# Performance work log

Measured on AMD Instinct MI355X. Metric: run time of the kernel, lower is better.

The kernel has to match this reference:

```python
import jax, jax.numpy as jnp
import numpy as np

N = 50000        # nodes
E = 800000       # edges (edge-nodes of the line graph)
LGE = 1600000    # line-graph edges
F_NODE = 256     # node feature dim
T = 64           # timestamp/edge feature dim
HID = 128        # hidden size
OUT = 64         # out size
SLOPE = 0.2      # leaky relu negative slope used in EdgeGCN / attention


def _glorot(key, shape):
    lim = jnp.sqrt(6.0 / (shape[0] + shape[1]))
    return jax.random.uniform(key, shape, jnp.float32, -lim, lim)


def setup_inputs() -> dict:
    key = jax.random.key(0)
    ks = jax.random.split(key, 24)
    inp = {
        "x": jax.random.normal(ks[0], (N, F_NODE), jnp.float32),
        "et": jax.random.normal(ks[1], (E, T), jnp.float32),
        "H": jax.random.randint(ks[2], (2, E), 0, N),
        "raw_edge_index": jax.random.randint(ks[3], (2, E), 0, N),
        "lg_edge_index": jax.random.randint(ks[4], (2, LGE), 0, E),
        # TSAEncoder: two SAGE-style layers on the line graph (T->HID->HID)
        "W_tsa1_s": _glorot(ks[5], (T, HID)),
        "W_tsa1_n": _glorot(ks[6], (T, HID)),
        "W_tsa2_s": _glorot(ks[7], (HID, HID)),
        "W_tsa2_n": _glorot(ks[8], (HID, HID)),
        # EdgeToNodeConv + EdgeGCN output linear
        "W_etn": _glorot(ks[9], (HID, HID)),
        "W_eg_lin": _glorot(ks[10], (HID, HID)),
        # edge_aggr SAGE (num_layers-1 = 1 layer)
        "W_ea_s": _glorot(ks[11], (HID, HID)),
        "W_ea_n": _glorot(ks[12], (HID, HID)),
        # attr_node_model SAGE (2 layers)
        "W_an1_s": _glorot(ks[13], (F_NODE, HID)),
        "W_an1_n": _glorot(ks[14], (F_NODE, HID)),
        "W_an2_s": _glorot(ks[15], (HID, HID)),
        "W_an2_n": _glorot(ks[16], (HID, HID)),
        # MixAttention
        "Wq": _glorot(ks[17], (HID, HID)),
        "Wk": _glorot(ks[18], (HID, HID)),
        "Wv": _glorot(ks[19], (HID, HID)),
        # final classifier
        "W_out": _glorot(ks[20], (HID, OUT)),
    }
    return inp


def _sage(h, src, dst, Ws, Wn, n):
    # mean-aggregator SAGE conv: self transform + mean of in-neighbors
    deg = jnp.clip(jax.ops.segment_sum(jnp.ones(src.shape[0], h.dtype), dst, num_segments=n), 1.0)
    nbr = jax.ops.segment_sum(h[src], dst, num_segments=n) / deg[:, None]
    return h @ Ws + nbr @ Wn


def reference(x, et, H, raw_edge_index, lg_edge_index,
              W_tsa1_s, W_tsa1_n, W_tsa2_s, W_tsa2_n,
              W_etn, W_eg_lin, W_ea_s, W_ea_n,
              W_an1_s, W_an1_n, W_an2_s, W_an2_n,
              Wq, Wk, Wv, W_out):
    src_lg, dst_lg = lg_edge_index[0], lg_edge_index[1]
    src, dst = raw_edge_index[0], raw_edge_index[1]

    # ---- EdgeGCN: TSAEncoder over line graph (edges as nodes) ----
    h = jax.nn.relu(_sage(et, src_lg, dst_lg, W_tsa1_s, W_tsa1_n, E))
    h = _sage(h, src_lg, dst_lg, W_tsa2_s, W_tsa2_n, E)          # [E, HID]

    # ---- EdgeToNodeConv: scatter edge reprs to both incident nodes (mean) ----
    ones_e = jnp.ones(E, h.dtype)
    agg = (jax.ops.segment_sum(h, H[0], num_segments=N)
           + jax.ops.segment_sum(h, H[1], num_segments=N))        # [N, HID]
    deg = jnp.clip(jax.ops.segment_sum(ones_e, H[0], num_segments=N)
                   + jax.ops.segment_sum(ones_e, H[1], num_segments=N), 1.0)
    node_e = (agg / deg[:, None]) @ W_etn
    edge_repr = jax.nn.leaky_relu(node_e, negative_slope=SLOPE) @ W_eg_lin  # [N, HID]

    # ---- edge_aggr: 1-layer SAGE over raw graph ----
    aggr_edge = _sage(edge_repr, src, dst, W_ea_s, W_ea_n, N)     # [N, HID]

    # ---- attr_node_model: 2-layer SAGE ----
    hn = jax.nn.relu(_sage(x, src, dst, W_an1_s, W_an1_n, N))
    hn = _sage(hn, src, dst, W_an2_s, W_an2_n, N)                 # [N, HID]

    # ---- MixAttention: edge-indexed cross attention (node queries, edge-repr keys/values) ----
    q = hn @ Wq
    k = aggr_edge @ Wk
    v = aggr_edge @ Wv
    score = jax.nn.leaky_relu(
        jnp.sum(q[dst] * k[src], axis=-1) / jnp.sqrt(jnp.asarray(HID, q.dtype)),
        negative_slope=SLOPE)                                     # [E]
    m = jax.ops.segment_max(score, dst, num_segments=N)
    m = jnp.where(jnp.isfinite(m), m, 0.0)
    ex = jnp.exp(score - m[dst])
    den = jnp.clip(jax.ops.segment_sum(ex, dst, num_segments=N), 1e-9)
    alpha = ex / den[dst]
    out = hn + jax.ops.segment_sum(alpha[:, None] * v[src], dst, num_segments=N)

    return jax.nn.log_softmax(out @ W_out, axis=1)                # [N, OUT]
```

## Files before the change

kernel.cpp:

```cpp
#include <hip/hip_runtime.h>
#include <cstddef>

static constexpr int Nn   = 50000;
static constexpr int Ee   = 800000;
static constexpr int LGEe = 1600000;

typedef __attribute__((ext_vector_type(8))) short bf16x8;
typedef __attribute__((ext_vector_type(4))) float f32x4;

__device__ __forceinline__ float bf2f(unsigned int u16) {
  return __uint_as_float(u16 << 16);
}
__device__ __forceinline__ unsigned int f2bf(float f) {
  unsigned int u = __float_as_uint(f);
  u += 0x7fffu + ((u >> 16) & 1u);
  return u >> 16;
}

__global__ __launch_bounds__(256)
void k_count_direct(const int* __restrict__ idx, int* __restrict__ cnt, int n) {
  int i = blockIdx.x * 256 + threadIdx.x;
  if (i < n) atomicAdd(&cnt[idx[i]], 1);
}
__global__ __launch_bounds__(256)
void k_scan1(const int* __restrict__ in, int* __restrict__ out,
             int* __restrict__ bsum, int n) {
  __shared__ int sd[256];
  int tid = threadIdx.x;
  int base = blockIdx.x * 1024 + tid * 4;
  int4 v = {0, 0, 0, 0};
  if (base < n) v = *(const int4*)(in + base);
  int s = v.x + v.y + v.z + v.w;
  sd[tid] = s; __syncthreads();
  for (int off = 1; off < 256; off <<= 1) {
    int t_ = (tid >= off) ? sd[tid - off] : 0; __syncthreads();
    sd[tid] += t_; __syncthreads();
  }
  int excl = sd[tid] - s;
  if (base < n) {
    int4 o; o.x = excl; o.y = o.x + v.x; o.z = o.y + v.y; o.w = o.z + v.z;
    *(int4*)(out + base) = o;
  }
  if (tid == 255) bsum[blockIdx.x] = sd[255];
}
__global__ __launch_bounds__(1024)
void k_scan2(int* __restrict__ b, int nb) {
  __shared__ int sd[1024];
  int tid = threadIdx.x;
  int v = (tid < nb) ? b[tid] : 0;
  sd[tid] = v; __syncthreads();
  for (int off = 1; off < 1024; off <<= 1) {
    int t_ = (tid >= off) ? sd[tid - off] : 0; __syncthreads();
    sd[tid] += t_; __syncthreads();
  }
  if (tid < nb) b[tid] = sd[tid] - v;
}
__global__ __launch_bounds__(256)
void k_scan3(int* __restrict__ out, const int* __restrict__ bsum, int n, int total,
             int* __restrict__ cur) {
  int i = blockIdx.x * 256 + threadIdx.x;
  if (i < n) {
    int v = out[i] + bsum[i >> 10];
    out[i] = v;
    cur[i] = v;
  }
  if (i == 0) out[n] = total;
}
__global__ __launch_bounds__(256)
void k_fillA(const int* __restrict__ dlg, const int* __restrict__ slg,
             int* __restrict__ cur, int* __restrict__ ent, int n) {
  int m = blockIdx.x * 256 + threadIdx.x;
  if (m >= n) return;
  int pos = atomicAdd(&cur[dlg[m]], 1);
  ent[pos] = slg[m];
}
__global__ __launch_bounds__(256)
void k_fillC2(const int* __restrict__ H, int* __restrict__ cur,
              int* __restrict__ ent, int n2, int E) {
  int i = blockIdx.x * 256 + threadIdx.x;
  if (i >= n2) return;
  int pos = atomicAdd(&cur[H[i]], 1);
  ent[pos] = (i >= E) ? i - E : i;
}
__global__ __launch_bounds__(256)
void k_fillD(const int* __restrict__ dstA, const int* __restrict__ srcA,
             int* __restrict__ cur, int* __restrict__ ent, int n) {
  int e = blockIdx.x * 256 + threadIdx.x;
  if (e >= n) return;
  int pos = atomicAdd(&cur[dstA[e]], 1);
  ent[pos] = srcA[e];
}
__global__ __launch_bounds__(256)
void k_rdeg(const int* __restrict__ ptr, float* __restrict__ r, int n) {
  int i = blockIdx.x * 256 + threadIdx.x;
  if (i < n) r[i] = 1.0f / fmaxf((float)(ptr[i + 1] - ptr[i]), 1.0f);
}

#define MG_SWEEP(WP, ACC)                                                       \
  {                                                                             \
    bf16x8 Bh[2][4], Bl[2][4];                                                  \
    _Pragma("unroll")                                                           \
    for (int np = 0; np < 2; ++np) {                                            \
      int n = (wv * 2 + np) * 16 + nrow;                                        \
      _Pragma("unroll")                                                         \
      for (int kc = 0; kc < 4; ++kc) {                                          \
        int kr0 = kh * 128 + kc * 32 + kg * 8;                                  \
        _Pragma("unroll")                                                       \
        for (int j = 0; j < 8; ++j) {                                           \
          float w = (WP)[(size_t)(kr0 + j) * 128 + n];                          \
          unsigned int hi = __float_as_uint(w) >> 16;                           \
          float lo = w - bf2f(hi);                                              \
          Bh[np][kc][j] = (short)(unsigned short)hi;                            \
          Bl[np][kc][j] = (short)(unsigned short)(__float_as_uint(lo) >> 16);   \
        }                                                                       \
      }                                                                         \
    }                                                                           \
    _Pragma("unroll")                                                           \
    for (int kc = 0; kc < 4; ++kc) {                                            \
      _Pragma("unroll")                                                         \
      for (int m = 0; m < 4; ++m) {                                             \
        int ss = m * 16 + nrow;                                                 \
        int idx = ss * 128 + ((kc * 32 + kg * 8) ^ ((ss & 7) << 3));            \
        bf16x8 ah = *(const bf16x8*)(sAh + idx);                                \
        bf16x8 al = *(const bf16x8*)(sAl + idx);                                \
        _Pragma("unroll")                                                       \
        for (int np = 0; np < 2; ++np) {                                        \
          ACC[m][np] = __builtin_amdgcn_mfma_f32_16x16x32_bf16(ah, Bh[np][kc], ACC[m][np], 0, 0, 0); \
          ACC[m][np] = __builtin_amdgcn_mfma_f32_16x16x32_bf16(al, Bh[np][kc], ACC[m][np], 0, 0, 0); \
          ACC[m][np] = __builtin_amdgcn_mfma_f32_16x16x32_bf16(ah, Bl[np][kc], ACC[m][np], 0, 0, 0); \
        }                                                                       \
      }                                                                         \
    }                                                                           \
  }

template <int DUAL>
__global__ __launch_bounds__(256)
void k_mgemm(int M, const float* __restrict__ A, int K,
             const float* __restrict__ W1, const float* __restrict__ W2,
             const float* __restrict__ dgA, int reluA, int act,
             float* __restrict__ C1, float* __restrict__ C2, int beta1)
{
  __shared__ __align__(16) unsigned char smem[34816];
  unsigned short* sAh = (unsigned short*)smem;
  unsigned short* sAl = (unsigned short*)(smem + 16384);
  float* stage = (float*)smem;

  const int t = threadIdx.x, wv = t >> 6;
  const int tr = t >> 4, tc = t & 15;
  const int nrow = (t & 63) & 15, kg = (t & 63) >> 4;
  const int row0 = blockIdx.x * 64;

  f32x4 acc1[4][2], acc2[4][2];
  #pragma unroll
  for (int m = 0; m < 4; ++m)
    #pragma unroll
    for (int np = 0; np < 2; ++np) {
      acc1[m][np] = (f32x4){0.f, 0.f, 0.f, 0.f};
      if (DUAL) acc2[m][np] = (f32x4){0.f, 0.f, 0.f, 0.f};
    }

  const int nkh = K >> 7;
  #pragma unroll 1
  for (int kh = 0; kh < nkh; ++kh) {
    if (kh) __syncthreads();
    #pragma unroll
    for (int j = 0; j < 8; ++j) {
      int idx = t + j * 256;
      int r = idx >> 5, c4 = idx & 31;
      int gr = row0 + r; if (gr > M - 1) gr = M - 1;
      float4 va = *(const float4*)(A + (size_t)gr * K + kh * 128 + c4 * 4);
      if (reluA) {
        va.x = fmaxf(va.x, 0.f); va.y = fmaxf(va.y, 0.f);
        va.z = fmaxf(va.z, 0.f); va.w = fmaxf(va.w, 0.f);
      }
      if (dgA) {
        float sc = dgA[gr];
        va.x *= sc; va.y *= sc; va.z *= sc; va.w *= sc;
      }
      float v[4] = {va.x, va.y, va.z, va.w};
      unsigned int h[4], l[4];
      #pragma unroll
      for (int q = 0; q < 4; ++q) {
        h[q] = __float_as_uint(v[q]) >> 16;
        l[q] = __float_as_uint(v[q] - bf2f(h[q])) >> 16;
      }
      int bidx = r * 128 + ((c4 * 4) ^ ((r & 7) << 3));
      uint2 ph = {h[0] | (h[1] << 16), h[2] | (h[3] << 16)};
      uint2 pl = {l[0] | (l[1] << 16), l[2] | (l[3] << 16)};
      *(uint2*)(sAh + bidx) = ph;
      *(uint2*)(sAl + bidx) = pl;
    }
    __syncthreads();

    MG_SWEEP(W1, acc1);
    if (DUAL) MG_SWEEP(W2, acc2);
  }

  __syncthreads();
  #pragma unroll
  for (int m = 0; m < 4; ++m)
    #pragma unroll
    for (int np = 0; np < 2; ++np)
      #pragma unroll
      for (int r = 0; r < 4; ++r)
        stage[(m * 16 + kg * 4 + r) * 132 + (wv * 2 + np) * 16 + nrow] = acc1[m][np][r];
  __syncthreads();
  #pragma unroll
  for (int i = 0; i < 4; ++i) {
    int s = tr * 4 + i, gr = row0 + s;
    if (gr >= M) continue;
    const float* sp = stage + s * 132 + tc * 8;
    float4 v0 = *(const float4*)sp, v1 = *(const float4*)(sp + 4);
    float o[8] = {v0.x, v0.y, v0.z, v0.w, v1.x, v1.y, v1.z, v1.w};
    #pragma unroll
    for (int j2 = 0; j2 < 8; ++j2) {
      float vv = o[j2];
      if (act == 1)      vv = fmaxf(vv, 0.f);
      else if (act == 2) vv = vv > 0.f ? vv : 0.2f * vv;
      o[j2] = vv;
    }
    float* p = C1 + (size_t)gr * 128 + tc * 8;
    if (beta1) {
      float4 c0 = *(const float4*)p, c1 = *(const float4*)(p + 4);
      o[0] += c0.x; o[1] += c0.y; o[2] += c0.z; o[3] += c0.w;
      o[4] += c1.x; o[5] += c1.y; o[6] += c1.z; o[7] += c1.w;
    }
    *(float4*)p       = *(const float4*)&o[0];
    *(float4*)(p + 4) = *(const float4*)&o[4];
  }
  if (DUAL) {
    __syncthreads();
    #pragma unroll
    for (int m = 0; m < 4; ++m)
      #pragma unroll
      for (int np = 0; np < 2; ++np)
        #pragma unroll
        for (int r = 0; r < 4; ++r)
          stage[(m * 16 + kg * 4 + r) * 132 + (wv * 2 + np) * 16 + nrow] = acc2[m][np][r];
    __syncthreads();
    #pragma unroll
    for (int i = 0; i < 4; ++i) {
      int s = tr * 4 + i, gr = row0 + s;
      if (gr >= M) continue;
      const float* sp = stage + s * 132 + tc * 8;
      float4 v0 = *(const float4*)sp, v1 = *(const float4*)(sp + 4);
      float o[8] = {v0.x, v0.y, v0.z, v0.w, v1.x, v1.y, v1.z, v1.w};
      #pragma unroll
      for (int j2 = 0; j2 < 8; ++j2) {
        float vv = o[j2];
        if (act == 1)      vv = fmaxf(vv, 0.f);
        else if (act == 2) vv = vv > 0.f ? vv : 0.2f * vv;
        o[j2] = vv;
      }
      float* p = C2 + (size_t)gr * 128 + tc * 8;
      *(float4*)p       = *(const float4*)&o[0];
      *(float4*)(p + 4) = *(const float4*)&o[4];
    }
  }
}

__global__ __launch_bounds__(256)
void k_tsa1(const float* __restrict__ et,
            const int* __restrict__ rp, const int* __restrict__ ent,
            const float* __restrict__ Ws, const float* __restrict__ Wn,
            unsigned short* __restrict__ BUF)
{
  __shared__ __align__(16) unsigned char smem[34816];
  unsigned short* sAh = (unsigned short*)smem;
  unsigned short* sAl = (unsigned short*)(smem + 16384);
  int*   sEnt  = (int*)(smem + 32768);
  float* stage = (float*)smem;

  const int t = threadIdx.x, wv = t >> 6, lane = t & 63;
  const int tr = t >> 4, tc = t & 15;
  const int nrow = lane & 15, kg = lane >> 4;
  const int seg0 = blockIdx.x * 64;
  const int segbase = seg0 + wv * 16;

  int rpv = (lane <= 16) ? rp[segbase + lane] : 0;
  int nxtv = __shfl(rpv, (lane + 1) & 63);
  float invv = 1.f / fmaxf((float)(nxtv - rpv), 1.f);

  const int base = rp[seg0];
  const int cnt  = rp[seg0 + 64] - base;
  const int lim  = cnt < 512 ? cnt : 512;
  for (int i = t; i < lim; i += 256) sEnt[i] = ent[base + i];

  {
    float dv[16];
    #pragma unroll
    for (int i = 0; i < 16; ++i)
      dv[i] = et[(size_t)(segbase + i) * 64 + lane];
    #pragma unroll
    for (int i = 0; i < 16; ++i) {
      int ss = wv * 16 + i;
      unsigned int hi = __float_as_uint(dv[i]) >> 16;
      float lo = dv[i] - bf2f(hi);
      int idx = ss * 128 + (lane ^ ((ss & 7) << 3));
      sAh[idx] = (unsigned short)hi;
      sAl[idx] = (unsigned short)(__float_as_uint(lo) >> 16);
    }
  }

  bf16x8 Bh[2][4], Bl[2][4];
  #pragma unroll
  for (int np = 0; np < 2; ++np) {
    int n = (wv * 2 + np) * 16 + nrow;
    #pragma unroll
    for (int kc = 0; kc < 4; ++kc) {
      const float* Wp = (kc < 2) ? Ws : Wn;
      int kr0 = (kc & 1) * 32 + kg * 8;
      #pragma unroll
      for (int j = 0; j < 8; ++j) {
        float w = Wp[(size_t)(kr0 + j) * 128 + n];
        unsigned int hi = __float_as_uint(w) >> 16;
        float lo = w - bf2f(hi);
        Bh[np][kc][j] = (short)(unsigned short)hi;
        Bl[np][kc][j] = (short)(unsigned short)(__float_as_uint(lo) >> 16);
      }
    }
  }
  __syncthreads();

  {
    int q0 = __shfl(rpv, 0);
    int q1 = __shfl(rpv, 16);
    int c = 0;
    int b_next = __shfl(rpv, 1);
    float idg = __shfl(invv, 0);
    float a = 0.f;
    #pragma unroll 1
    for (int j = q0; j < q1; j += 8) {
      float x[8];
      #pragma unroll
      for (int u = 0; u < 8; ++u) {
        int jj = j + u; jj = jj < q1 ? jj : q1 - 1;
        int ix = jj - base;
        int s = (ix < 512) ? sEnt[ix] : ent[jj];
        x[u] = et[(size_t)s * 64 + lane];
      }
      #pragma unroll
      for (int u = 0; u < 8; ++u) {
        int jj = j + u;
        if (jj >= q1) break;
        while (jj >= b_next) {
          float v = a * idg;
          int ss = wv * 16 + c;
          unsigned int hi = __float_as_uint(v) >> 16;
          float lo = v - bf2f(hi);
          int idx = ss * 128 + ((64 + lane) ^ ((ss & 7) << 3));
          sAh[idx] = (unsigned short)hi;
          sAl[idx] = (unsigned short)(__float_as_uint(lo) >> 16);
          a = 0.f;
          ++c;
          b_next = __shfl(rpv, c + 1);
          idg = __shfl(invv, c);
        }
        a += x[u];
      }
    }
    #pragma unroll 1
    for (;;) {
      float v = a * idg;
      int ss = wv * 16 + c;
      unsigned int hi = __float_as_uint(v) >> 16;
      float lo = v - bf2f(hi);
      int idx = ss * 128 + ((64 + lane) ^ ((ss & 7) << 3));
      sAh[idx] = (unsigned short)hi;
      sAl[idx] = (unsigned short)(__float_as_uint(lo) >> 16);
      a = 0.f;
      if (++c >= 16) break;
      idg = __shfl(invv, c);
    }
  }
  __syncthreads();

  f32x4 acc[4][2];
  #pragma unroll
  for (int m = 0; m < 4; ++m)
    #pragma unroll
    for (int np = 0; np < 2; ++np)
      acc[m][np] = (f32x4){0.f, 0.f, 0.f, 0.f};

  #pragma unroll
  for (int kc = 0; kc < 4; ++kc) {
    #pragma unroll
    for (int m = 0; m < 4; ++m) {
      int ss = m * 16 + nrow;
      int kbase = kc * 32 + kg * 8;
      int idx = ss * 128 + (kbase ^ ((ss & 7) << 3));
      bf16x8 ah = *(const bf16x8*)(sAh + idx);
      bf16x8 al = *(const bf16x8*)(sAl + idx);
      #pragma unroll
      for (int np = 0; np < 2; ++np) {
        acc[m][np] = __builtin_amdgcn_mfma_f32_16x16x32_bf16(ah, Bh[np][kc], acc[m][np], 0, 0, 0);
        acc[m][np] = __builtin_amdgcn_mfma_f32_16x16x32_bf16(al, Bh[np][kc], acc[m][np], 0, 0, 0);
        acc[m][np] = __builtin_amdgcn_mfma_f32_16x16x32_bf16(ah, Bl[np][kc], acc[m][np], 0, 0, 0);
      }
    }
  }

  __syncthreads();
  #pragma unroll
  for (int m = 0; m < 4; ++m)
    #pragma unroll
    for (int np = 0; np < 2; ++np)
      #pragma unroll
      for (int r = 0; r < 4; ++r)
        stage[(m * 16 + kg * 4 + r) * 132 + (wv * 2 + np) * 16 + nrow] = acc[m][np][r];
  __syncthreads();
  #pragma unroll
  for (int i = 0; i < 4; ++i) {
    int s = tr * 4 + i;
    const float* sp = stage + s * 132 + tc * 8;
    float4 v0 = *(const float4*)sp;
    float4 v1 = *(const float4*)(sp + 4);
    unsigned int pk[4];
    pk[0] = f2bf(v0.x) | (f2bf(v0.y) << 16);
    pk[1] = f2bf(v0.z) | (f2bf(v0.w) << 16);
    pk[2] = f2bf(v1.x) | (f2bf(v1.y) << 16);
    pk[3] = f2bf(v1.z) | (f2bf(v1.w) << 16);
    uint4 st = {pk[0], pk[1], pk[2], pk[3]};
    *(uint4*)(BUF + (size_t)(seg0 + s) * 128 + tc * 8) = st;
  }
}

__global__ __launch_bounds__(256)
void k_pool12(const int* __restrict__ rp, const int* __restrict__ ent,
              const int* __restrict__ rpA, const int* __restrict__ entA,
              const unsigned short* __restrict__ BUF,
              float* __restrict__ OS, float* __restrict__ ON,
              int nseg, int total)
{
  const int wv = threadIdx.x >> 6, lane = threadIdx.x & 63;
  const int chunk = blockIdx.x * 4 + wv;
  const int c0 = chunk * 128;
  if (c0 >= total) return;
  int c1 = c0 + 128; if (c1 > total) c1 = total;

  int lo = 0, hi = nseg;
  while (lo + 1 < hi) {
    int mid = (lo + hi) >> 1;
    if (rp[mid] <= c0) lo = mid; else hi = mid;
  }
  int seg = lo;
  int sstart = rp[seg];
  int send = rp[seg + 1];
  float s0 = 0.f, s1 = 0.f, n0 = 0.f, n1 = 0.f;

  #pragma unroll 1
  for (int j = c0; j < c1; j += 8) {
    int ids[8];
    #pragma unroll
    for (int u = 0; u < 8; ++u) {
      int jj = j + u; jj = jj < c1 ? jj : c1 - 1;
      ids[u] = ent[jj];
    }
    unsigned int uv[8];
    int pA0[8], pA1[8];
    #pragma unroll
    for (int u = 0; u < 8; ++u)
      uv[u] = *(const unsigned int*)(BUF + (size_t)ids[u] * 128 + 2 * lane);
    #pragma unroll
    for (int u = 0; u < 8; ++u) { pA0[u] = rpA[ids[u]]; pA1[u] = rpA[ids[u] + 1]; }
    #pragma unroll
    for (int u = 0; u < 8; ++u) {
      int jj = j + u;
      if (jj >= c1) break;
      while (jj >= send) {
        float* pS = OS + (size_t)seg * 128;
        float* pN = ON + (size_t)seg * 128;
        if (sstart >= c0 && send <= c1) {
          pS[2 * lane]     += s0;  pS[2 * lane + 1] += s1;
          pN[2 * lane]     += n0;  pN[2 * lane + 1] += n1;
        } else {
          atomicAdd(pS + 2 * lane, s0);     atomicAdd(pS + 2 * lane + 1, s1);
          atomicAdd(pN + 2 * lane, n0);     atomicAdd(pN + 2 * lane + 1, n1);
        }
        s0 = s1 = n0 = n1 = 0.f;
        ++seg; sstart = send; send = rp[seg + 1];
      }
      s0 += fmaxf(bf2f(uv[u] & 0xffffu), 0.f);
      s1 += fmaxf(bf2f(uv[u] >> 16),     0.f);
      int p0 = pA0[u], p1 = pA1[u];
      float a0 = 0.f, a1 = 0.f;
      #pragma unroll 1
      for (int t2 = p0; t2 < p1; t2 += 4) {
        unsigned int w[4];
        int rem = p1 - t2;
        #pragma unroll
        for (int v2 = 0; v2 < 4; ++v2)
          if (v2 < rem)
            w[v2] = *(const unsigned int*)(BUF + (size_t)entA[t2 + v2] * 128 + 2 * lane);
        #pragma unroll
        for (int v2 = 0; v2 < 4; ++v2)
          if (v2 < rem) {
            a0 += fmaxf(bf2f(w[v2] & 0xffffu), 0.f);
            a1 += fmaxf(bf2f(w[v2] >> 16),     0.f);
          }
      }
      float idg = 1.f / fmaxf((float)(p1 - p0), 1.f);
      n0 += a0 * idg; n1 += a1 * idg;
    }
  }
  {
    float* pS = OS + (size_t)seg * 128;
    float* pN = ON + (size_t)seg * 128;
    if (sstart >= c0 && send <= c1) {
      pS[2 * lane]     += s0;  pS[2 * lane + 1] += s1;
      pN[2 * lane]     += n0;  pN[2 * lane + 1] += n1;
    } else {
      atomicAdd(pS + 2 * lane, s0);     atomicAdd(pS + 2 * lane + 1, s1);
      atomicAdd(pN + 2 * lane, n0);     atomicAdd(pN + 2 * lane + 1, n1);
    }
  }
}

__global__ __launch_bounds__(256)
void k_poolf(const int* __restrict__ rp, const int* __restrict__ ent,
             const float* __restrict__ SRC, float* __restrict__ O,
             int nseg, int total)
{
  const int wv = threadIdx.x >> 6, lane = threadIdx.x & 63;
  const int chunk = blockIdx.x * 4 + wv;
  const int c0 = chunk * 256;
  if (c0 >= total) return;
  int c1 = c0 + 256; if (c1 > total) c1 = total;

  int lo = 0, hi = nseg;
  while (lo + 1 < hi) {
    int mid = (lo + hi) >> 1;
    if (rp[mid] <= c0) lo = mid; else hi = mid;
  }
  int seg = lo;
  int sstart = rp[seg];
  int send = rp[seg + 1];
  float a0 = 0.f, a1 = 0.f;

  #pragma unroll 1
  for (int j = c0; j < c1; j += 8) {
    int ids[8];
    #pragma unroll
    for (int u = 0; u < 8; ++u) {
      int jj = j + u; jj = jj < c1 ? jj : c1 - 1;
      ids[u] = ent[jj];
    }
    float2 v[8];
    #pragma unroll
    for (int u = 0; u < 8; ++u)
      v[u] = ((const float2*)(SRC + (size_t)ids[u] * 128))[lane];
    #pragma unroll
    for (int u = 0; u < 8; ++u) {
      int jj = j + u;
      if (jj >= c1) break;
      while (jj >= send) {
        float sc = 1.f / fmaxf((float)(send - sstart), 1.f);
        float* p = O + (size_t)seg * 128;
        if (sstart >= c0 && send <= c1) {
          p[2 * lane]     += a0 * sc;
          p[2 * lane + 1] += a1 * sc;
        } else {
          atomicAdd(p + 2 * lane, a0 * sc);
          atomicAdd(p + 2 * lane + 1, a1 * sc);
        }
        a0 = a1 = 0.f;
        ++seg; sstart = send; send = rp[seg + 1];
      }
      a0 += v[u].x; a1 += v[u].y;
    }
  }
  {
    float sc = 1.f / fmaxf((float)(send - sstart), 1.f);
    float* p = O + (size_t)seg * 128;
    if (sstart >= c0 && send <= c1) {
      p[2 * lane]     += a0 * sc;
      p[2 * lane + 1] += a1 * sc;
    } else {
      atomicAdd(p + 2 * lane, a0 * sc);
      atomicAdd(p + 2 * lane + 1, a1 * sc);
    }
  }
}

__global__ __launch_bounds__(256)
void k_attn(const int* __restrict__ rp, const int* __restrict__ ent,
            const float* __restrict__ q, const float* __restrict__ kb,
            const float* __restrict__ vb, float* __restrict__ o, int nseg)
{
  int wv = threadIdx.x >> 6, lane = threadIdx.x & 63;
  int seg = blockIdx.x * 4 + wv;
  if (seg >= nseg) return;
  int p0 = rp[seg], p1 = rp[seg + 1];
  if (p0 >= p1) return;
  float2 q2 = ((const float2*)(q + (size_t)seg * 128))[lane];
  float m = -1e30f, l = 0.f, o0 = 0.f, o1 = 0.f;
  #pragma unroll 1
  for (int j = p0; j < p1; j += 4) {
    int s[4];
    #pragma unroll
    for (int i = 0; i < 4; ++i) {
      int jj = j + i; jj = jj < p1 ? jj : p1 - 1;
      s[i] = ent[jj];
    }
    float2 k2[4], v2[4];
    #pragma unroll
    for (int i = 0; i < 4; ++i)
      k2[i] = ((const float2*)(kb + (size_t)s[i] * 128))[lane];
    #pragma unroll
    for (int i = 0; i < 4; ++i)
      v2[i] = ((const float2*)(vb + (size_t)s[i] * 128))[lane];
    float d[4];
    #pragma unroll
    for (int i = 0; i < 4; ++i) d[i] = fmaf(q2.x, k2[i].x, q2.y * k2[i].y);
    #pragma unroll
    for (int off = 1; off < 64; off <<= 1) {
      #pragma unroll
      for (int i = 0; i < 4; ++i) d[i] += __shfl_xor(d[i], off);
    }
    float sc[4];
    #pragma unroll
    for (int i = 0; i < 4; ++i) {
      float v = d[i] * 0.088388347648318447f;
      v = v > 0.f ? v : 0.2f * v;
      sc[i] = (j + i < p1) ? v : -1e30f;
    }
    float mb = fmaxf(fmaxf(sc[0], sc[1]), fmaxf(sc[2], sc[3]));
    float mn = fmaxf(m, mb);
    float scale = expf(m - mn);
    float e[4];
    #pragma unroll
    for (int i = 0; i < 4; ++i)
      e[i] = (j + i < p1) ? expf(sc[i] - mn) : 0.f;
    l  = l  * scale + ((e[0] + e[1]) + (e[2] + e[3]));
    o0 = o0 * scale + ((e[0] * v2[0].x + e[1] * v2[1].x) + (e[2] * v2[2].x + e[3] * v2[3].x));
    o1 = o1 * scale + ((e[0] * v2[0].y + e[1] * v2[1].y) + (e[2] * v2[2].y + e[3] * v2[3].y));
    m = mn;
  }
  float inv = 1.f / fmaxf(l, 1e-9f);
  float2* orow = (float2*)(o + (size_t)seg * 128);
  float2 cur = orow[lane];
  cur.x += o0 * inv; cur.y += o1 * inv;
  orow[lane] = cur;
}

__global__ __launch_bounds__(256)
void k_out(const float* __restrict__ attn, const float* __restrict__ Wout,
           float* __restrict__ out, int n) {
  __shared__ float sW[128 * 64];
  for (int i = threadIdx.x; i < 128 * 64; i += 256) sW[i] = Wout[i];
  __syncthreads();
  int wave = threadIdx.x >> 6, lane = threadIdx.x & 63;
  int row = blockIdx.x * 4 + wave;
  if (row >= n) return;
  const float* a = attn + (size_t)row * 128;
  float z = 0.f;
  #pragma unroll 8
  for (int k = 0; k < 128; ++k) z = fmaf(a[k], sW[k * 64 + lane], z);
  float mx = z;
  #pragma unroll
  for (int off = 32; off; off >>= 1) mx = fmaxf(mx, __shfl_xor(mx, off));
  float ee = expf(z - mx);
  float ss = ee;
  #pragma unroll
  for (int off = 32; off; off >>= 1) ss += __shfl_xor(ss, off);
  out[(size_t)row * 64 + lane] = z - mx - logf(ss);
}

extern "C" void kernel_launch(void* const* d_in, const int* in_sizes, int n_in,
                              void* d_out, int out_size, void* d_ws, size_t ws_size,
                              hipStream_t stream) {
  (void)in_sizes; (void)n_in; (void)out_size;
  const float* x        = (const float*)d_in[0];
  const float* et       = (const float*)d_in[1];
  const int*   H0       = (const int*)d_in[2];
  const int*   src      = (const int*)d_in[3];
  const int*   dst      = src + Ee;
  const int*   src_lg   = (const int*)d_in[4];
  const int*   dst_lg   = src_lg + LGEe;
  const float* W_tsa1_s = (const float*)d_in[5];
  const float* W_tsa1_n = (const float*)d_in[6];
  const float* W_tsa2_s = (const float*)d_in[7];
  const float* W_tsa2_n = (const float*)d_in[8];
  const float* W_etn    = (const float*)d_in[9];
  const float* W_eg_lin = (const float*)d_in[10];
  const float* W_ea_s   = (const float*)d_in[11];
  const float* W_ea_n   = (const float*)d_in[12];
  const float* W_an1_s  = (const float*)d_in[13];
  const float* W_an1_n  = (const float*)d_in[14];
  const float* W_an2_s  = (const float*)d_in[15];
  const float* W_an2_n  = (const float*)d_in[16];
  const float* Wq       = (const float*)d_in[17];
  const float* Wk       = (const float*)d_in[18];
  const float* Wv       = (const float*)d_in[19];
  const float* W_out    = (const float*)d_in[20];
  float* out = (float*)d_out;

  char* wp = (char*)d_ws;
  size_t avail = ws_size;
  auto alloc = [&](size_t bytes) -> void* {
    void* r = (void*)wp;
    size_t pad = (bytes + 255) & ~(size_t)255;
    wp += pad; avail = (avail >= pad) ? avail - pad : 0;
    return r;
  };
  const size_t NH = (size_t)Nn * 128;
  unsigned short* BUF = (unsigned short*)alloc((size_t)Ee * 128 * 2);
  float* aggN  = (float*)alloc(NH * 4);
  float* aggS  = (float*)alloc(NH * 4);
  int* ptrA  = (int*)alloc(((size_t)Ee + 1) * 4);
  int* cntA  = (int*)alloc((size_t)Ee * 4);
  int* entA  = (int*)alloc((size_t)LGEe * 4);
  int* ptrC  = (int*)alloc(((size_t)Nn + 1) * 4);
  int* cntC  = (int*)alloc((size_t)Nn * 4);
  int* entC  = (int*)alloc((size_t)2 * Ee * 4);
  int* ptrD  = (int*)alloc(((size_t)Nn + 1) * 4);
  int* cntD  = (int*)alloc((size_t)Nn * 4);
  int* entD  = (int*)alloc((size_t)Ee * 4);
  float* rdegN = (float*)alloc((size_t)Nn * 4);
  int* bsum  = (int*)alloc(2048 * 4);
  if (avail == 0 && wp > (char*)d_ws + ws_size) return;

  float* er  = (float*)BUF + 0 * NH;
  float* ae  = (float*)BUF + 1 * NH;
  float* hn  = (float*)BUF + 2 * NH;
  float* hn2 = (float*)BUF + 3 * NH;
  float* qb  = (float*)BUF + 4 * NH;
  float* kb  = (float*)BUF + 5 * NH;
  float* vb  = (float*)BUF + 6 * NH;
  float* tmp = (float*)BUF + 7 * NH;

  auto cdiv = [](long a, long b) { return (int)((a + b - 1) / b); };
  auto scan = [&](int* cnt, int* ptr, int n, int total) {
    int nb = cdiv(n, 1024);
    k_scan1<<<nb, 256, 0, stream>>>(cnt, ptr, bsum, n);
    k_scan2<<<1, 1024, 0, stream>>>(bsum, nb);
    k_scan3<<<cdiv(n, 256), 256, 0, stream>>>(ptr, bsum, n, total, cnt);
  };

  const int gLG = cdiv(LGEe, 256), gEe = cdiv(Ee, 256), g2E = cdiv(2 * Ee, 256);

  hipMemsetAsync(cntA, 0, (size_t)Ee * 4, stream);
  k_count_direct<<<gLG, 256, 0, stream>>>(dst_lg, cntA, LGEe);
  scan(cntA, ptrA, Ee, LGEe);
  k_fillA<<<gLG, 256, 0, stream>>>(dst_lg, src_lg, cntA, entA, LGEe);

  hipMemsetAsync(cntC, 0, (size_t)Nn * 4, stream);
  k_count_direct<<<g2E, 256, 0, stream>>>(H0, cntC, 2 * Ee);
  scan(cntC, ptrC, Nn, 2 * Ee);
  k_fillC2<<<g2E, 256, 0, stream>>>(H0, cntC, entC, 2 * Ee, Ee);

  hipMemsetAsync(cntD, 0, (size_t)Nn * 4, stream);
  k_count_direct<<<gEe, 256, 0, stream>>>(dst, cntD, Ee);
  scan(cntD, ptrD, Nn, Ee);
  k_fillD<<<gEe, 256, 0, stream>>>(dst, src, cntD, entD, Ee);
  k_rdeg<<<cdiv(Nn, 256), 256, 0, stream>>>(ptrC, rdegN, Nn);

  const int gM64  = cdiv(Nn, 64);
  const int gW    = cdiv(Nn, 4);
  const int gP12  = cdiv(cdiv(2 * Ee, 128), 4);
  const int gPf   = cdiv(cdiv(Ee, 256), 4);

  k_tsa1<<<Ee / 64, 256, 0, stream>>>(et, ptrA, entA, W_tsa1_s, W_tsa1_n, BUF);

  hipMemsetAsync(aggS, 0, NH * 4, stream);
  hipMemsetAsync(aggN, 0, NH * 4, stream);
  k_pool12<<<gP12, 256, 0, stream>>>(ptrC, entC, ptrA, entA, BUF, aggS, aggN, Nn, 2 * Ee);
  k_mgemm<0><<<gM64, 256, 0, stream>>>(Nn, aggN, 128, W_tsa2_n, nullptr, nullptr, 0, 0, aggN, nullptr, 0);
  k_mgemm<0><<<gM64, 256, 0, stream>>>(Nn, aggS, 128, W_tsa2_s, nullptr, nullptr, 0, 0, aggN, nullptr, 1);
  k_mgemm<0><<<gM64, 256, 0, stream>>>(Nn, aggN, 128, W_etn, nullptr, rdegN, 0, 2, tmp, nullptr, 0);
  k_mgemm<0><<<gM64, 256, 0, stream>>>(Nn, tmp, 128, W_eg_lin, nullptr, nullptr, 0, 0, er, nullptr, 0);

  k_mgemm<1><<<gM64, 256, 0, stream>>>(Nn, er, 128, W_ea_s, W_ea_n, nullptr, 0, 0, ae, tmp, 0);
  k_poolf<<<gPf, 256, 0, stream>>>(ptrD, entD, tmp, ae, Nn, Ee);

  k_mgemm<1><<<gM64, 256, 0, stream>>>(Nn, x, 256, W_an1_s, W_an1_n, nullptr, 0, 0, hn, tmp, 0);
  k_poolf<<<gPf, 256, 0, stream>>>(ptrD, entD, tmp, hn, Nn, Ee);
  k_mgemm<1><<<gM64, 256, 0, stream>>>(Nn, hn, 128, W_an2_s, W_an2_n, nullptr, 1, 0, hn2, tmp, 0);
  k_poolf<<<gPf, 256, 0, stream>>>(ptrD, entD, tmp, hn2, Nn, Ee);

  k_mgemm<0><<<gM64, 256, 0, stream>>>(Nn, hn2, 128, Wq, nullptr, nullptr, 0, 0, qb, nullptr, 0);
  k_mgemm<1><<<gM64, 256, 0, stream>>>(Nn, ae, 128, Wk, Wv, nullptr, 0, 0, kb, vb, 0);
  k_attn<<<gW, 256, 0, stream>>>(ptrD, entD, qb, kb, vb, hn2, Nn);

  k_out<<<gW, 256, 0, stream>>>(hn2, W_out, out, Nn);
}
```

Measured before the change: 2.356 ms.

## Precompute flattened composed CSR for two-hop neighbor pooling with per-entry weights

Replaces the nested two-level gather in the fused pool kernel, which walked each incident edge's line-graph neighbor list, with a precomputed CSR that maps each node directly to line-graph source edges, each carrying a 1/deg weight. Pooling then becomes two flat weighted segment-sum passes using a single generic kernel. This removes the irregular inner loop and its load imbalance. In exchange it adds a count/scan/fill pass over 3.2M entries with atomics, plus about 25MB of extra index and weight arrays.

```diff
diff --git a/kernel.cpp b/kernel.cpp
--- a/kernel.cpp
+++ b/kernel.cpp
@@ -21,6 +21,15 @@
 void k_count_direct(const int* __restrict__ idx, int* __restrict__ cnt, int n) {
   int i = blockIdx.x * 256 + threadIdx.x;
   if (i < n) atomicAdd(&cnt[idx[i]], 1);
+}
+__global__ __launch_bounds__(256)
+void k_count_comp2(const int* __restrict__ H, const int* __restrict__ dlg,
+                   int* __restrict__ cnt, int n2, int LGE, int E) {
+  int i = blockIdx.x * 256 + threadIdx.x;
+  if (i >= n2) return;
+  int b = i >= LGE;
+  int m = b ? i - LGE : i;
+  atomicAdd(&cnt[H[b * E + dlg[m]]], 1);
 }
 __global__ __launch_bounds__(256)
 void k_scan1(const int* __restrict__ in, int* __restrict__ out,
@@ -73,6 +82,21 @@
   if (m >= n) return;
   int pos = atomicAdd(&cur[dlg[m]], 1);
   ent[pos] = slg[m];
+}
+__global__ __launch_bounds__(256)
+void k_fillB2(const int* __restrict__ H, const int* __restrict__ dlg,
+              const int* __restrict__ slg, const int* __restrict__ ptrA,
+              int* __restrict__ cur, int* __restrict__ entS,
+              float* __restrict__ entW, int n2, int LGE, int E) {
+  int i = blockIdx.x * 256 + threadIdx.x;
+  if (i >= n2) return;
+  int b = i >= LGE;
+  int m = b ? i - LGE : i;
+  int d = dlg[m];
+  int pos = atomicAdd(&cur[H[b * E + d]], 1);
+  entS[pos] = slg[m];
+  int la = ptrA[d + 1] - ptrA[d];
+  entW[pos] = 1.0f / (float)max(la, 1);
 }
 __global__ __launch_bounds__(256)
 void k_fillC2(const int* __restrict__ H, int* __restrict__ cur,
@@ -426,17 +450,16 @@
 }
 
 __global__ __launch_bounds__(256)
-void k_pool12(const int* __restrict__ rp, const int* __restrict__ ent,
-              const int* __restrict__ rpA, const int* __restrict__ entA,
-              const unsigned short* __restrict__ BUF,
-              float* __restrict__ OS, float* __restrict__ ON,
-              int nseg, int total)
+void k_poolb(const int* __restrict__ rp, const int* __restrict__ ent,
+             const float* __restrict__ entw,
+             const unsigned short* __restrict__ SRC,
+             float* __restrict__ O, int nseg, int total)
 {
   const int wv = threadIdx.x >> 6, lane = threadIdx.x & 63;
   const int chunk = blockIdx.x * 4 + wv;
-  const int c0 = chunk * 128;
+  const int c0 = chunk * 256;
   if (c0 >= total) return;
-  int c1 = c0 + 128; if (c1 > total) c1 = total;
+  int c1 = c0 + 256; if (c1 > total) c1 = total;
 
   int lo = 0, hi = nseg;
   while (lo + 1 < hi) {
@@ -446,72 +469,49 @@
   int seg = lo;
   int sstart = rp[seg];
   int send = rp[seg + 1];
-  float s0 = 0.f, s1 = 0.f, n0 = 0.f, n1 = 0.f;
+  float a0 = 0.f, a1 = 0.f;
 
   #pragma unroll 1
   for (int j = c0; j < c1; j += 8) {
-    int ids[8];
+    int ids[8]; float w[8];
     #pragma unroll
     for (int u = 0; u < 8; ++u) {
       int jj = j + u; jj = jj < c1 ? jj : c1 - 1;
       ids[u] = ent[jj];
+      w[u] = entw ? entw[jj] : 1.f;
     }
     unsigned int uv[8];
-    int pA0[8], pA1[8];
     #pragma unroll
     for (int u = 0; u < 8; ++u)
-      uv[u] = *(const unsigned int*)(BUF + (size_t)ids[u] * 128 + 2 * lane);
-    #pragma unroll
-    for (int u = 0; u < 8; ++u) { pA0[u] = rpA[ids[u]]; pA1[u] = rpA[ids[u] + 1]; }
+      uv[u] = *(const unsigned int*)(SRC + (size_t)ids[u] * 128 + 2 * lane);
     #pragma unroll
     for (int u = 0; u < 8; ++u) {
       int jj = j + u;
       if (jj >= c1) break;
       while (jj >= send) {
-        float* pS = OS + (size_t)seg * 128;
-        float* pN = ON + (size_t)seg * 128;
+        float* p = O + (size_t)seg * 128;
         if (sstart >= c0 && send <= c1) {
-          pS[2 * lane]     += s0;  pS[2 * lane + 1] += s1;
-          pN[2 * lane]     += n0;  pN[2 * lane + 1] += n1;
+          p[2 * lane]     += a0;
+          p[2 * lane + 1] += a1;
         } else {
-          atomicAdd(pS + 2 * lane, s0);     atomicAdd(pS + 2 * lane + 1, s1);
-          atomicAdd(pN + 2 * lane, n0);     atomicAdd(pN + 2 * lane + 1, n1);
+          atomicAdd(p + 2 * lane, a0);
+          atomicAdd(p + 2 * lane + 1, a1);
         }
-        s0 = s1 = n0 = n1 = 0.f;
+        a0 = a1 = 0.f;
         ++seg; sstart = send; send = rp[seg + 1];
       }
-      s0 += fmaxf(bf2f(uv[u] & 0xffffu), 0.f);
-      s1 += fmaxf(bf2f(uv[u] >> 16),     0.f);
-      int p0 = pA0[u], p1 = pA1[u];
-      float a0 = 0.f, a1 = 0.f;
-      #pragma unroll 1
-      for (int t2 = p0; t2 < p1; t2 += 4) {
-        unsigned int w[4];
-        int rem = p1 - t2;
-        #pragma unroll
-        for (int v2 = 0; v2 < 4; ++v2)
-          if (v2 < rem)
-            w[v2] = *(const unsigned int*)(BUF + (size_t)entA[t2 + v2] * 128 + 2 * lane);
-        #pragma unroll
-        for (int v2 = 0; v2 < 4; ++v2)
-          if (v2 < rem) {
-            a0 += fmaxf(bf2f(w[v2] & 0xffffu), 0.f);
-            a1 += fmaxf(bf2f(w[v2] >> 16),     0.f);
-          }
-      }
-      float idg = 1.f / fmaxf((float)(p1 - p0), 1.f);
-      n0 += a0 * idg; n1 += a1 * idg;
+      a0 = fmaf(w[u], fmaxf(bf2f(uv[u] & 0xffffu), 0.f), a0);
+      a1 = fmaf(w[u], fmaxf(bf2f(uv[u] >> 16),     0.f), a1);
     }
   }
   {
-    float* pS = OS + (size_t)seg * 128;
-    float* pN = ON + (size_t)seg * 128;
+    float* p = O + (size_t)seg * 128;
     if (sstart >= c0 && send <= c1) {
-      pS[2 * lane]     += s0;  pS[2 * lane + 1] += s1;
-      pN[2 * lane]     += n0;  pN[2 * lane + 1] += n1;
+      p[2 * lane]     += a0;
+      p[2 * lane + 1] += a1;
     } else {
-      atomicAdd(pS + 2 * lane, s0);     atomicAdd(pS + 2 * lane + 1, s1);
-      atomicAdd(pN + 2 * lane, n0);     atomicAdd(pN + 2 * lane + 1, n1);
+      atomicAdd(p + 2 * lane, a0);
+      atomicAdd(p + 2 * lane + 1, a1);
     }
   }
 }
@@ -710,6 +710,10 @@
   int* ptrA  = (int*)alloc(((size_t)Ee + 1) * 4);
   int* cntA  = (int*)alloc((size_t)Ee * 4);
   int* entA  = (int*)alloc((size_t)LGEe * 4);
+  int* ptrB  = (int*)alloc(((size_t)Nn + 1) * 4);
+  int* cntB  = (int*)alloc((size_t)Nn * 4);
+  int* entBs = (int*)alloc((size_t)2 * LGEe * 4);
+  float* entBw = (float*)alloc((size_t)2 * LGEe * 4);
   int* ptrC  = (int*)alloc(((size_t)Nn + 1) * 4);
   int* cntC  = (int*)alloc((size_t)Nn * 4);
   int* entC  = (int*)alloc((size_t)2 * Ee * 4);
@@ -737,12 +741,19 @@
     k_scan3<<<cdiv(n, 256), 256, 0, stream>>>(ptr, bsum, n, total, cnt);
   };
 
-  const int gLG = cdiv(LGEe, 256), gEe = cdiv(Ee, 256), g2E = cdiv(2 * Ee, 256);
+  const int gLG = cdiv(LGEe, 256), gEe = cdiv(Ee, 256);
+  const int g2E = cdiv(2 * Ee, 256), g2LG = cdiv(2 * LGEe, 256);
 
   hipMemsetAsync(cntA, 0, (size_t)Ee * 4, stream);
   k_count_direct<<<gLG, 256, 0, stream>>>(dst_lg, cntA, LGEe);
   scan(cntA, ptrA, Ee, LGEe);
   k_fillA<<<gLG, 256, 0, stream>>>(dst_lg, src_lg, cntA, entA, LGEe);
+
+  hipMemsetAsync(cntB, 0, (size_t)Nn * 4, stream);
+  k_count_comp2<<<g2LG, 256, 0, stream>>>(H0, dst_lg, cntB, 2 * LGEe, LGEe, Ee);
+  scan(cntB, ptrB, Nn, 2 * LGEe);
+  k_fillB2<<<g2LG, 256, 0, stream>>>(H0, dst_lg, src_lg, ptrA, cntB, entBs, entBw,
+                                     2 * LGEe, LGEe, Ee);
 
   hipMemsetAsync(cntC, 0, (size_t)Nn * 4, stream);
   k_count_direct<<<g2E, 256, 0, stream>>>(H0, cntC, 2 * Ee);
@@ -757,14 +768,16 @@
 
   const int gM64  = cdiv(Nn, 64);
   const int gW    = cdiv(Nn, 4);
-  const int gP12  = cdiv(cdiv(2 * Ee, 128), 4);
+  const int gP2   = cdiv(cdiv(2 * LGEe, 256), 4);
+  const int gP1   = cdiv(cdiv(2 * Ee, 256), 4);
   const int gPf   = cdiv(cdiv(Ee, 256), 4);
 
   k_tsa1<<<Ee / 64, 256, 0, stream>>>(et, ptrA, entA, W_tsa1_s, W_tsa1_n, BUF);
 
+  hipMemsetAsync(aggN, 0, NH * 4, stream);
   hipMemsetAsync(aggS, 0, NH * 4, stream);
-  hipMemsetAsync(aggN, 0, NH * 4, stream);
-  k_pool12<<<gP12, 256, 0, stream>>>(ptrC, entC, ptrA, entA, BUF, aggS, aggN, Nn, 2 * Ee);
+  k_poolb<<<gP2, 256, 0, stream>>>(ptrB, entBs, entBw, BUF, aggN, Nn, 2 * LGEe);
+  k_poolb<<<gP1, 256, 0, stream>>>(ptrC, entC, nullptr, BUF, aggS, Nn, 2 * Ee);
   k_mgemm<0><<<gM64, 256, 0, stream>>>(Nn, aggN, 128, W_tsa2_n, nullptr, nullptr, 0, 0, aggN, nullptr, 0);
   k_mgemm<0><<<gM64, 256, 0, stream>>>(Nn, aggS, 128, W_tsa2_s, nullptr, nullptr, 0, 0, aggN, nullptr, 1);
   k_mgemm<0><<<gM64, 256, 0, stream>>>(Nn, aggN, 128, W_etn, nullptr, rdegN, 0, 2, tmp, nullptr, 0);
```

Result: no change. 2.331 ms (-1.1%).
